# Kernel tuning notes

Measured on AMD Instinct MI355X. Metric: run time of the kernel, lower is better.

Reference implementation:

```python
import jax, jax.numpy as jnp
import numpy as np

B, N, D = 2, 2048, 512
H, VD = 8, 64  # v_dim = hid_dim / n_head


def setup_inputs() -> dict:
    key = jax.random.key(0)
    k1, k2, k3, k4 = jax.random.split(key, 4)
    inputs = jax.random.normal(k1, (B, N, D), dtype=jnp.float32)
    # lecun_normal: std = 1/sqrt(fan_in) with fan_in = D
    s = 1.0 / np.sqrt(D)
    q_w = jax.random.normal(k2, (H, D, VD), dtype=jnp.float32) * s
    k_w = jax.random.normal(k3, (H, D, VD), dtype=jnp.float32) * s
    v_w = jax.random.normal(k4, (H, D, VD), dtype=jnp.float32) * s
    return {"inputs": inputs, "q_w": q_w, "k_w": k_w, "v_w": v_w}


def reference(inputs, q_w, k_w, v_w):
    # QKV projections: [B,N,D] x [H,D,VD] -> [B,H,N,VD]
    q = jnp.einsum('bnj,hjk->bhnk', inputs, q_w)
    k = jnp.einsum('bnj,hjk->bhnk', inputs, k_w)
    v = jnp.einsum('bnj,hjk->bhnk', inputs, v_w)
    scale = 1.0 / jnp.sqrt(jnp.asarray(VD, dtype=q.dtype))
    scores = jnp.einsum('bhik,bhjk->bhij', q, k) * scale  # [B,H,N,N]
    att = jax.nn.softmax(scores, axis=-1)
    out = jnp.einsum('bhnj,bhjd->bhnd', att, v)  # [B,H,N,VD]
    out = jnp.transpose(out, (0, 2, 1, 3)).reshape(inputs.shape[0], -1, H * VD)  # [B,N,hid_dim]
    # keras GELU default is exact (non-approximate)
    return jax.nn.gelu(out, approximate=False)
```

## Files before the change

kernel.cpp:

```cpp
#include <hip/hip_runtime.h>
#include <hip/hip_bf16.h>
#include <math.h>

#define BB 2
#define NN 2048
#define DD 512
#define HH 8
#define VD 64

typedef _Float16 half8 __attribute__((ext_vector_type(8)));
typedef _Float16 half4 __attribute__((ext_vector_type(4)));
typedef __fp16 fp16x2 __attribute__((ext_vector_type(2)));
typedef float f32x4 __attribute__((ext_vector_type(4)));

#define GLDS16(gp, lp) __builtin_amdgcn_global_load_lds( \
    (const __attribute__((address_space(1))) void*)(gp), \
    (__attribute__((address_space(3))) void*)(lp), 16, 0, 0)

__device__ __forceinline__ float fexp2(float x) {
#if __has_builtin(__builtin_amdgcn_exp2f)
    return __builtin_amdgcn_exp2f(x);
#else
    return exp2f(x);
#endif
}

__device__ __forceinline__ void stage8(const _Float16* gsrc, size_t ldg, int r0,
                                       _Float16* lbase, int lane) {
    int r8 = lane >> 3;
    int ce = ((lane & 7) ^ r8) << 3;
    const _Float16* g = gsrc + (size_t)(r0 + r8) * ldg + ce;
    GLDS16(g, lbase);
}

__device__ __forceinline__ half8 frag_ld(const _Float16* tile, int row, int cb) {
    int off = row * 128 + (cb ^ ((row & 7) << 4));
    return *(const half8*)((const char*)tile + off);
}

__device__ __forceinline__ half8 frag_ldv(const _Float16* tile, int row, int cb) {
    int off = row * 256 + (cb ^ ((row & 15) << 4));
    return *(const half8*)((const char*)tile + off);
}

__device__ __forceinline__ float gelu_exact(float v) {
    return 0.5f * v * (1.f + erff(v * 0.70710678118654752f));
}

#define SM_BYTES 66560

__global__ __launch_bounds__(256) void k_prep(
    const float* __restrict__ x,
    const float* __restrict__ qw, const float* __restrict__ kw,
    const float* __restrict__ vw,
    _Float16* __restrict__ wt, _Float16* __restrict__ xh)
{
    __shared__ __align__(16) float ls[64][65];
    const int bid = blockIdx.x, t = threadIdx.x;
#pragma unroll
    for (int j = 0; j < 2; ++j) {
        size_t idx = (((size_t)bid * 2 + j) * 256 + t) * 8;
        float4 a = *(const float4*)(x + idx);
        float4 b = *(const float4*)(x + idx + 4);
        half8 hv;
        hv[0] = (_Float16)a.x; hv[1] = (_Float16)a.y;
        hv[2] = (_Float16)a.z; hv[3] = (_Float16)a.w;
        hv[4] = (_Float16)b.x; hv[5] = (_Float16)b.y;
        hv[6] = (_Float16)b.z; hv[7] = (_Float16)b.w;
        *(half8*)(xh + idx) = hv;
    }
    if (bid < 192) {
        const int kc = bid & 7, h = (bid >> 3) & 7, ty = bid >> 6;
        const float* src = (ty == 0) ? qw : (ty == 1) ? kw : vw;
#pragma unroll
        for (int j = 0; j < 4; ++j) {
            int idx = t + 256 * j;
            int k = idx >> 4, o4 = idx & 15;
            float4 v = *(const float4*)(src + ((size_t)(h * DD + kc * 64 + k) * VD + o4 * 4));
            ls[k][o4 * 4 + 0] = v.x; ls[k][o4 * 4 + 1] = v.y;
            ls[k][o4 * 4 + 2] = v.z; ls[k][o4 * 4 + 3] = v.w;
        }
        __syncthreads();
#pragma unroll
        for (int j = 0; j < 4; ++j) {
            int idx = t + 256 * j;
            int o = idx >> 4, k4 = idx & 15;
            half4 hv;
#pragma unroll
            for (int i = 0; i < 4; ++i) hv[i] = (_Float16)ls[k4 * 4 + i][o];
            *(half4*)(wt + ((size_t)(ty * HH + h) * VD + o) * DD + kc * 64 + k4 * 4) = hv;
        }
    }
}

__global__ __launch_bounds__(256) void k_proj(
    const _Float16* __restrict__ xh,
    const _Float16* __restrict__ wt,
    _Float16* __restrict__ qsp,
    _Float16* __restrict__ kbp,
    _Float16* __restrict__ vtp)
{
    __shared__ __align__(16) _Float16 xls[2][4096];
    __shared__ __align__(16) _Float16 wls[2][12288];
    const int bid = blockIdx.x, t = threadIdx.x;
    const int wave = t >> 6, lane = t & 63;
    const int lq = lane & 15, g = lane >> 4;
    const int h = bid & 7;
    const int m0 = (bid >> 3) * 64;
    const int rbase = 32 * (wave >> 1);
    const int cbase = 96 * (wave & 1);

    f32x4 acc[2][6];
#pragma unroll
    for (int a = 0; a < 2; ++a)
#pragma unroll
        for (int c = 0; c < 6; ++c) acc[a][c] = (f32x4){0.f, 0.f, 0.f, 0.f};

    auto stage = [&](int buf, int ks) {
#pragma unroll
        for (int j = 0; j < 2; ++j) {
            int i = wave * 2 + j;
            stage8(xh + (size_t)m0 * DD + ks * 64, DD, i * 8, &xls[buf][i * 512], lane);
        }
#pragma unroll
        for (int j = 0; j < 6; ++j) {
            int i = wave * 6 + j;
            int ty = i >> 3;
            int ol = (i & 7) * 8;
            stage8(wt + ((size_t)(ty * HH + h) * VD + ol) * DD + ks * 64, DD, 0,
                   &wls[buf][i * 512], lane);
        }
    };

    stage(0, 0);
    stage(1, 1);
    for (int ks = 0; ks < 8; ++ks) {
        const int buf = ks & 1;
        if (ks < 7) asm volatile("s_waitcnt vmcnt(8)" ::: "memory");
        else        asm volatile("s_waitcnt vmcnt(0)" ::: "memory");
        __builtin_amdgcn_s_barrier();
        half8 af[2][2];
        half8 bf[6][2];
#pragma unroll
        for (int amt = 0; amt < 2; ++amt) {
            af[amt][0] = frag_ld(xls[buf], rbase + amt * 16 + lq, 16 * g);
            af[amt][1] = frag_ld(xls[buf], rbase + amt * 16 + lq, 64 + 16 * g);
        }
#pragma unroll
        for (int ct = 0; ct < 6; ++ct) {
            int wr = cbase + ct * 16 + lq;
            bf[ct][0] = frag_ld(wls[buf], wr, 16 * g);
            bf[ct][1] = frag_ld(wls[buf], wr, 64 + 16 * g);
        }
        asm volatile("s_waitcnt lgkmcnt(0)" ::: "memory");
        __builtin_amdgcn_sched_barrier(0);
        __builtin_amdgcn_s_barrier();
        if (ks + 2 < 8) stage(buf, ks + 2);
        __builtin_amdgcn_s_setprio(1);
#pragma unroll
        for (int ct = 0; ct < 6; ++ct) {
#pragma unroll
            for (int amt = 0; amt < 2; ++amt) {
                acc[amt][ct] = __builtin_amdgcn_mfma_f32_16x16x32_f16(af[amt][0], bf[ct][0], acc[amt][ct], 0, 0, 0);
                acc[amt][ct] = __builtin_amdgcn_mfma_f32_16x16x32_f16(af[amt][1], bf[ct][1], acc[amt][ct], 0, 0, 0);
            }
        }
        __builtin_amdgcn_s_setprio(0);
    }

    const int b0 = m0 >> 11;
    const int nb0 = m0 & (NN - 1);
    const size_t bh = (size_t)(b0 * HH + h);
    _Float16* ldsA = &wls[0][0];
    _Float16* ldsV = &wls[0][0];
    const int rn = t >> 2;
    const int rc = t & 3;

    __syncthreads();
    if ((wave & 1) == 0) {
#pragma unroll
        for (int ct = 0; ct < 4; ++ct) {
            int o = ct * 16 + lq;
#pragma unroll
            for (int amt = 0; amt < 2; ++amt)
#pragma unroll
                for (int i = 0; i < 4; ++i) {
                    int n = rbase + amt * 16 + 4 * g + i;
                    ldsA[n * 72 + o] = (_Float16)(acc[amt][ct][i] * 0.18033688011112042f);
                }
        }
    }
    __syncthreads();
    {
        half8 v0 = *(const half8*)&ldsA[rn * 72 + rc * 16];
        half8 v1 = *(const half8*)&ldsA[rn * 72 + rc * 16 + 8];
        _Float16* qp = qsp + (bh * NN + nb0 + rn) * VD + rc * 16;
        *(half8*)qp = v0;
        *(half8*)(qp + 8) = v1;
    }

    __syncthreads();
    if ((wave & 1) == 0) {
#pragma unroll
        for (int ct = 4; ct < 6; ++ct) {
            int o = (ct - 4) * 16 + lq;
#pragma unroll
            for (int amt = 0; amt < 2; ++amt)
#pragma unroll
                for (int i = 0; i < 4; ++i) {
                    int n = rbase + amt * 16 + 4 * g + i;
                    ldsA[n * 72 + o] = (_Float16)acc[amt][ct][i];
                }
        }
    } else {
#pragma unroll
        for (int ct = 0; ct < 2; ++ct) {
            int o = 32 + ct * 16 + lq;
#pragma unroll
            for (int amt = 0; amt < 2; ++amt)
#pragma unroll
                for (int i = 0; i < 4; ++i) {
                    int n = rbase + amt * 16 + 4 * g + i;
                    ldsA[n * 72 + o] = (_Float16)acc[amt][ct][i];
                }
        }
    }
    __syncthreads();
    {
        half8 v0 = *(const half8*)&ldsA[rn * 72 + rc * 16];
        half8 v1 = *(const half8*)&ldsA[rn * 72 + rc * 16 + 8];
        _Float16* kp = kbp + (bh * NN + nb0 + rn) * VD + rc * 16;
        *(half8*)kp = v0;
        *(half8*)(kp + 8) = v1;
    }

    __syncthreads();
    if (wave & 1) {
#pragma unroll
        for (int ct = 2; ct < 6; ++ct) {
            int o = (ct - 2) * 16 + lq;
#pragma unroll
            for (int amt = 0; amt < 2; ++amt) {
                int n0 = rbase + amt * 16 + 4 * g;
                half4 hv;
#pragma unroll
                for (int i = 0; i < 4; ++i) hv[i] = (_Float16)acc[amt][ct][i];
                *(half4*)&ldsV[o * 88 + n0] = hv;
            }
        }
    }
    __syncthreads();
    {
#pragma unroll
        for (int blk = 0; blk < 2; ++blk) {
            half4 lo = *(const half4*)&ldsV[rn * 88 + 32 * blk + 4 * rc];
            half4 hi = *(const half4*)&ldsV[rn * 88 + 32 * blk + 16 + 4 * rc];
            half8 pk;
            pk[0] = lo[0]; pk[1] = lo[1]; pk[2] = lo[2]; pk[3] = lo[3];
            pk[4] = hi[0]; pk[5] = hi[1]; pk[6] = hi[2]; pk[7] = hi[3];
            *(half8*)(vtp + (bh * VD + rn) * NN + nb0 + 32 * blk + 8 * rc) = pk;
        }
    }
}

__global__ __launch_bounds__(256, 2) void k_attn(
    const _Float16* __restrict__ qs,
    const _Float16* __restrict__ kb,
    const _Float16* __restrict__ vt,
    float* __restrict__ out)
{
    constexpr int NITER = NN / 128;
    __shared__ __align__(16) char SM[SM_BYTES];
    const int bid = blockIdx.x, t = threadIdx.x;
    const int wave = t >> 6, lane = t & 63;
    const int lq = lane & 15, g = lane >> 4;
    const int xcd = bid & 7;
    const int bh = xcd * 2 + ((bid >> 3) & 1);
    const int qt = bid >> 4;
    const int qbase = qt * 64;

    half8 qf[4][2];
#pragma unroll
    for (int qg = 0; qg < 4; ++qg)
#pragma unroll
        for (int ds = 0; ds < 2; ++ds)
            qf[qg][ds] = *(const half8*)(qs + ((size_t)bh * NN + qbase + 16 * qg + lq) * VD + 32 * ds + 8 * g);

    const int r8 = lane >> 3;
    const _Float16* kS = kb + ((size_t)bh * NN + 32 * wave + r8) * VD + 8 * ((lane & 7) ^ r8);
    const _Float16* vS[4];
#pragma unroll
    for (int uu = 0; uu < 4; ++uu) {
        int vrow = 16 * wave + 4 * uu + g;
        vS[uu] = vt + ((size_t)bh * VD + vrow) * NN + 8 * (lq ^ (vrow & 15));
    }

    _Float16* kb0 = (_Float16*)(SM);
    _Float16* vb0 = (_Float16*)(SM + 16384);
    _Float16* kb1 = (_Float16*)(SM + 32768);
    _Float16* vb1 = (_Float16*)(SM + 49152);

    auto stage = [&](int b, int j) {
        _Float16* kd = (b ? kb1 : kb0) + 4 * wave * 512;
        const _Float16* kp = kS + (size_t)j * 128 * VD;
#pragma unroll
        for (int uu = 0; uu < 4; ++uu)
            GLDS16(kp + uu * 8 * VD, kd + uu * 512);
        _Float16* vd = (b ? vb1 : vb0) + 4 * wave * 512;
#pragma unroll
        for (int uu = 0; uu < 4; ++uu)
            GLDS16(vS[uu] + j * 128, vd + uu * 512);
    };

    f32x4 oacc[4][4];
    f32x4 oacc_l[4];
#pragma unroll
    for (int qg = 0; qg < 4; ++qg) {
#pragma unroll
        for (int dt = 0; dt < 4; ++dt) oacc[qg][dt] = (f32x4){0.f, 0.f, 0.f, 0.f};
        oacc_l[qg] = (f32x4){0.f, 0.f, 0.f, 0.f};
    }
    half8 vones;
#pragma unroll
    for (int i = 0; i < 8; ++i) vones[i] = (_Float16)1.0f;

    stage(0, 0);
    stage(1, 1);

    union PU { fp16x2 h2[4]; half8 h8; };

    for (int j = 0; j < NITER; ++j) {
        const int b = j & 1;
        if (j < NITER - 1) asm volatile("s_waitcnt vmcnt(8)" ::: "memory");
        else               asm volatile("s_waitcnt vmcnt(0)" ::: "memory");
        __builtin_amdgcn_s_barrier();
        const _Float16* kB = b ? kb1 : kb0;
        const _Float16* vB = b ? vb1 : vb0;
        half8 kf[2][2], vf[4];
#pragma unroll
        for (int mt = 0; mt < 2; ++mt)
#pragma unroll
            for (int ds = 0; ds < 2; ++ds)
                kf[mt][ds] = frag_ld(kB, 32 * wave + 16 * mt + lq, 64 * ds + 16 * g);
#pragma unroll
        for (int dt = 0; dt < 4; ++dt)
            vf[dt] = frag_ldv(vB, 16 * dt + lq, 64 * wave + 16 * g);
        asm volatile("s_waitcnt lgkmcnt(0)" ::: "memory");
        __builtin_amdgcn_sched_barrier(0);
        __builtin_amdgcn_s_barrier();
        if (j + 2 < NITER) stage(b, j + 2);
        f32x4 sc[2][2];
        __builtin_amdgcn_s_setprio(1);
#pragma unroll
        for (int mt = 0; mt < 2; ++mt) {
            sc[0][mt] = (f32x4){0.f, 0.f, 0.f, 0.f};
            sc[0][mt] = __builtin_amdgcn_mfma_f32_16x16x32_f16(kf[mt][0], qf[0][0], sc[0][mt], 0, 0, 0);
            sc[0][mt] = __builtin_amdgcn_mfma_f32_16x16x32_f16(kf[mt][1], qf[0][1], sc[0][mt], 0, 0, 0);
        }
#pragma unroll
        for (int qg = 0; qg < 4; ++qg) {
            const int cur = qg & 1;
            if (qg < 3) {
#pragma unroll
                for (int mt = 0; mt < 2; ++mt) {
                    sc[cur ^ 1][mt] = (f32x4){0.f, 0.f, 0.f, 0.f};
                    sc[cur ^ 1][mt] = __builtin_amdgcn_mfma_f32_16x16x32_f16(kf[mt][0], qf[qg + 1][0], sc[cur ^ 1][mt], 0, 0, 0);
                    sc[cur ^ 1][mt] = __builtin_amdgcn_mfma_f32_16x16x32_f16(kf[mt][1], qf[qg + 1][1], sc[cur ^ 1][mt], 0, 0, 0);
                }
            }
            PU pu;
            {
                float p00 = fexp2(sc[cur][0][0]);
                float p01 = fexp2(sc[cur][0][1]);
                float p02 = fexp2(sc[cur][0][2]);
                float p03 = fexp2(sc[cur][0][3]);
                float p10 = fexp2(sc[cur][1][0]);
                float p11 = fexp2(sc[cur][1][1]);
                float p12 = fexp2(sc[cur][1][2]);
                float p13 = fexp2(sc[cur][1][3]);
                pu.h2[0] = __builtin_amdgcn_cvt_pkrtz(p00, p01);
                pu.h2[1] = __builtin_amdgcn_cvt_pkrtz(p02, p03);
                pu.h2[2] = __builtin_amdgcn_cvt_pkrtz(p10, p11);
                pu.h2[3] = __builtin_amdgcn_cvt_pkrtz(p12, p13);
            }
#pragma unroll
            for (int dt = 0; dt < 4; ++dt)
                oacc[qg][dt] = __builtin_amdgcn_mfma_f32_16x16x32_f16(vf[dt], pu.h8, oacc[qg][dt], 0, 0, 0);
            oacc_l[qg] = __builtin_amdgcn_mfma_f32_16x16x32_f16(vones, pu.h8, oacc_l[qg], 0, 0, 0);
        }
        __builtin_amdgcn_s_setprio(0);
    }

    float* lsm  = (float*)(SM + 65536);
    float* sred = (float*)SM;
    __syncthreads();
    if (g == 0) {
#pragma unroll
        for (int qg = 0; qg < 4; ++qg) lsm[wave * 64 + 16 * qg + lq] = oacc_l[qg][0];
    }
#pragma unroll
    for (int qg = 0; qg < 4; ++qg)
#pragma unroll
        for (int dt = 0; dt < 4; ++dt)
            *(f32x4*)(sred + (size_t)wave * 4096 + (16 * qg + lq) * 64 + 16 * dt + 4 * g) = oacc[qg][dt];
    __syncthreads();
    const int b2 = bh >> 3, h = bh & 7;
    const int q = t >> 2, cg2 = t & 3;
    float lt = (lsm[q] + lsm[64 + q]) + (lsm[128 + q] + lsm[192 + q]);
    float inv = 1.f / lt;
    float* op = out + ((size_t)b2 * NN + qbase + q) * (HH * VD) + h * VD + 16 * cg2;
#pragma unroll
    for (int c2 = 0; c2 < 4; ++c2) {
        int off = q * 64 + 16 * cg2 + 4 * c2;
        f32x4 o = *(const f32x4*)(sred + off);
        o += *(const f32x4*)(sred + 4096 + off);
        o += *(const f32x4*)(sred + 8192 + off);
        o += *(const f32x4*)(sred + 12288 + off);
        float4 r;
        r.x = gelu_exact(o[0] * inv);
        r.y = gelu_exact(o[1] * inv);
        r.z = gelu_exact(o[2] * inv);
        r.w = gelu_exact(o[3] * inv);
        *(float4*)(op + 4 * c2) = r;
    }
}

extern "C" void kernel_launch(void* const* d_in, const int* in_sizes, int n_in,
                              void* d_out, int out_size, void* d_ws, size_t ws_size,
                              hipStream_t stream)
{
    const float* x  = (const float*)d_in[0];
    const float* qw = (const float*)d_in[1];
    const float* kw = (const float*)d_in[2];
    const float* vw = (const float*)d_in[3];
    float* out = (float*)d_out;

    _Float16* wt  = (_Float16*)d_ws;
    _Float16* xhp = wt  + 786432;
    _Float16* qsp = xhp + 2097152;
    _Float16* kbp = qsp + 2097152;
    _Float16* vtp = kbp + 2097152;

    hipLaunchKernelGGL(k_prep, dim3(512), dim3(256), 0, stream,
                       x, qw, kw, vw, wt, xhp);
    hipLaunchKernelGGL(k_proj, dim3(512), dim3(256), 0, stream,
                       xhp, wt, qsp, kbp, vtp);
    hipLaunchKernelGGL(k_attn, dim3(512), dim3(256), 0, stream,
                       qsp, kbp, vtp, out);
}
```

Measured before the change: 49.96 us.

## Load K/V fragments directly from global into registers, dropping LDS staging

The attention main loop stops staging K and V tiles through LDS with global_load_lds and barriers. Each wave now loads its own K and V MFMA fragments straight from global memory into two register sets that alternate, and the loop is fully unrolled. This is meant to remove LDS round trips and the two block barriers per iteration. In exchange it uses more registers, issues smaller strided global loads whose latency must be hidden by the register double buffer, and loses the swizzled bank-conflict-free layout.

New measurement: 59.82 us. 1.2x slower.

```diff
diff --git a/kernel.cpp b/kernel.cpp
--- a/kernel.cpp
+++ b/kernel.cpp
@@ -35,11 +35,6 @@
 
 __device__ __forceinline__ half8 frag_ld(const _Float16* tile, int row, int cb) {
     int off = row * 128 + (cb ^ ((row & 7) << 4));
-    return *(const half8*)((const char*)tile + off);
-}
-
-__device__ __forceinline__ half8 frag_ldv(const _Float16* tile, int row, int cb) {
-    int off = row * 256 + (cb ^ ((row & 15) << 4));
     return *(const half8*)((const char*)tile + off);
 }
 
@@ -286,31 +281,8 @@
         for (int ds = 0; ds < 2; ++ds)
             qf[qg][ds] = *(const half8*)(qs + ((size_t)bh * NN + qbase + 16 * qg + lq) * VD + 32 * ds + 8 * g);
 
-    const int r8 = lane >> 3;
-    const _Float16* kS = kb + ((size_t)bh * NN + 32 * wave + r8) * VD + 8 * ((lane & 7) ^ r8);
-    const _Float16* vS[4];
-#pragma unroll
-    for (int uu = 0; uu < 4; ++uu) {
-        int vrow = 16 * wave + 4 * uu + g;
-        vS[uu] = vt + ((size_t)bh * VD + vrow) * NN + 8 * (lq ^ (vrow & 15));
-    }
-
-    _Float16* kb0 = (_Float16*)(SM);
-    _Float16* vb0 = (_Float16*)(SM + 16384);
-    _Float16* kb1 = (_Float16*)(SM + 32768);
-    _Float16* vb1 = (_Float16*)(SM + 49152);
-
-    auto stage = [&](int b, int j) {
-        _Float16* kd = (b ? kb1 : kb0) + 4 * wave * 512;
-        const _Float16* kp = kS + (size_t)j * 128 * VD;
-#pragma unroll
-        for (int uu = 0; uu < 4; ++uu)
-            GLDS16(kp + uu * 8 * VD, kd + uu * 512);
-        _Float16* vd = (b ? vb1 : vb0) + 4 * wave * 512;
-#pragma unroll
-        for (int uu = 0; uu < 4; ++uu)
-            GLDS16(vS[uu] + j * 128, vd + uu * 512);
-    };
+    const _Float16* kP = kb + ((size_t)bh * NN + 32 * wave + lq) * VD + 8 * g;
+    const _Float16* vP = vt + ((size_t)bh * VD + lq) * NN + 32 * wave + 8 * g;
 
     f32x4 oacc[4][4];
     f32x4 oacc_l[4];
@@ -324,72 +296,70 @@
 #pragma unroll
     for (int i = 0; i < 8; ++i) vones[i] = (_Float16)1.0f;
 
-    stage(0, 0);
-    stage(1, 1);
-
     union PU { fp16x2 h2[4]; half8 h8; };
 
-    for (int j = 0; j < NITER; ++j) {
-        const int b = j & 1;
-        if (j < NITER - 1) asm volatile("s_waitcnt vmcnt(8)" ::: "memory");
-        else               asm volatile("s_waitcnt vmcnt(0)" ::: "memory");
-        __builtin_amdgcn_s_barrier();
-        const _Float16* kB = b ? kb1 : kb0;
-        const _Float16* vB = b ? vb1 : vb0;
-        half8 kf[2][2], vf[4];
-#pragma unroll
-        for (int mt = 0; mt < 2; ++mt)
-#pragma unroll
-            for (int ds = 0; ds < 2; ++ds)
-                kf[mt][ds] = frag_ld(kB, 32 * wave + 16 * mt + lq, 64 * ds + 16 * g);
-#pragma unroll
-        for (int dt = 0; dt < 4; ++dt)
-            vf[dt] = frag_ldv(vB, 16 * dt + lq, 64 * wave + 16 * g);
-        asm volatile("s_waitcnt lgkmcnt(0)" ::: "memory");
-        __builtin_amdgcn_sched_barrier(0);
-        __builtin_amdgcn_s_barrier();
-        if (j + 2 < NITER) stage(b, j + 2);
-        f32x4 sc[2][2];
-        __builtin_amdgcn_s_setprio(1);
-#pragma unroll
-        for (int mt = 0; mt < 2; ++mt) {
-            sc[0][mt] = (f32x4){0.f, 0.f, 0.f, 0.f};
-            sc[0][mt] = __builtin_amdgcn_mfma_f32_16x16x32_f16(kf[mt][0], qf[0][0], sc[0][mt], 0, 0, 0);
-            sc[0][mt] = __builtin_amdgcn_mfma_f32_16x16x32_f16(kf[mt][1], qf[0][1], sc[0][mt], 0, 0, 0);
-        }
-#pragma unroll
-        for (int qg = 0; qg < 4; ++qg) {
-            const int cur = qg & 1;
-            if (qg < 3) {
-#pragma unroll
-                for (int mt = 0; mt < 2; ++mt) {
-                    sc[cur ^ 1][mt] = (f32x4){0.f, 0.f, 0.f, 0.f};
-                    sc[cur ^ 1][mt] = __builtin_amdgcn_mfma_f32_16x16x32_f16(kf[mt][0], qf[qg + 1][0], sc[cur ^ 1][mt], 0, 0, 0);
-                    sc[cur ^ 1][mt] = __builtin_amdgcn_mfma_f32_16x16x32_f16(kf[mt][1], qf[qg + 1][1], sc[cur ^ 1][mt], 0, 0, 0);
-                }
-            }
-            PU pu;
-            {
-                float p00 = fexp2(sc[cur][0][0]);
-                float p01 = fexp2(sc[cur][0][1]);
-                float p02 = fexp2(sc[cur][0][2]);
-                float p03 = fexp2(sc[cur][0][3]);
-                float p10 = fexp2(sc[cur][1][0]);
-                float p11 = fexp2(sc[cur][1][1]);
-                float p12 = fexp2(sc[cur][1][2]);
-                float p13 = fexp2(sc[cur][1][3]);
-                pu.h2[0] = __builtin_amdgcn_cvt_pkrtz(p00, p01);
-                pu.h2[1] = __builtin_amdgcn_cvt_pkrtz(p02, p03);
-                pu.h2[2] = __builtin_amdgcn_cvt_pkrtz(p10, p11);
-                pu.h2[3] = __builtin_amdgcn_cvt_pkrtz(p12, p13);
-            }
-#pragma unroll
-            for (int dt = 0; dt < 4; ++dt)
-                oacc[qg][dt] = __builtin_amdgcn_mfma_f32_16x16x32_f16(vf[dt], pu.h8, oacc[qg][dt], 0, 0, 0);
-            oacc_l[qg] = __builtin_amdgcn_mfma_f32_16x16x32_f16(vones, pu.h8, oacc_l[qg], 0, 0, 0);
-        }
-        __builtin_amdgcn_s_setprio(0);
-    }
+#define LOADK(DST, J)                                                            \
+    _Pragma("unroll") for (int mt = 0; mt < 2; ++mt)                             \
+        _Pragma("unroll") for (int ds = 0; ds < 2; ++ds)                         \
+            DST[mt][ds] = *(const half8*)(kP + ((size_t)(J) * 128 + mt * 16) * VD + ds * 32);
+
+#define LOADV(DST, J)                                                            \
+    _Pragma("unroll") for (int dt = 0; dt < 4; ++dt)                             \
+        DST[dt] = *(const half8*)(vP + (size_t)dt * 16 * NN + (J) * 128);
+
+#define AT_COMP(KF, VF)                                                          \
+    {                                                                            \
+        f32x4 sc[2][2];                                                          \
+        __builtin_amdgcn_s_setprio(1);                                           \
+        _Pragma("unroll") for (int mt = 0; mt < 2; ++mt) {                       \
+            sc[0][mt] = (f32x4){0.f, 0.f, 0.f, 0.f};                             \
+            sc[0][mt] = __builtin_amdgcn_mfma_f32_16x16x32_f16(KF[mt][0], qf[0][0], sc[0][mt], 0, 0, 0); \
+            sc[0][mt] = __builtin_amdgcn_mfma_f32_16x16x32_f16(KF[mt][1], qf[0][1], sc[0][mt], 0, 0, 0); \
+        }                                                                        \
+        _Pragma("unroll") for (int qg = 0; qg < 4; ++qg) {                       \
+            const int cur = qg & 1;                                              \
+            if (qg < 3) {                                                        \
+                _Pragma("unroll") for (int mt = 0; mt < 2; ++mt) {               \
+                    sc[cur ^ 1][mt] = (f32x4){0.f, 0.f, 0.f, 0.f};               \
+                    sc[cur ^ 1][mt] = __builtin_amdgcn_mfma_f32_16x16x32_f16(KF[mt][0], qf[qg + 1][0], sc[cur ^ 1][mt], 0, 0, 0); \
+                    sc[cur ^ 1][mt] = __builtin_amdgcn_mfma_f32_16x16x32_f16(KF[mt][1], qf[qg + 1][1], sc[cur ^ 1][mt], 0, 0, 0); \
+                }                                                                \
+            }                                                                    \
+            PU pu;                                                               \
+            {                                                                    \
+                float p00 = fexp2(sc[cur][0][0]);                                \
+                float p01 = fexp2(sc[cur][0][1]);                                \
+                float p02 = fexp2(sc[cur][0][2]);                                \
+                float p03 = fexp2(sc[cur][0][3]);                                \
+                float p10 = fexp2(sc[cur][1][0]);                                \
+                float p11 = fexp2(sc[cur][1][1]);                                \
+                float p12 = fexp2(sc[cur][1][2]);                                \
+                float p13 = fexp2(sc[cur][1][3]);                                \
+                pu.h2[0] = __builtin_amdgcn_cvt_pkrtz(p00, p01);                 \
+                pu.h2[1] = __builtin_amdgcn_cvt_pkrtz(p02, p03);                 \
+                pu.h2[2] = __builtin_amdgcn_cvt_pkrtz(p10, p11);                 \
+                pu.h2[3] = __builtin_amdgcn_cvt_pkrtz(p12, p13);                 \
+            }                                                                    \
+            _Pragma("unroll") for (int dt = 0; dt < 4; ++dt)                     \
+                oacc[qg][dt] = __builtin_amdgcn_mfma_f32_16x16x32_f16(VF[dt], pu.h8, oacc[qg][dt], 0, 0, 0); \
+            oacc_l[qg] = __builtin_amdgcn_mfma_f32_16x16x32_f16(vones, pu.h8, oacc_l[qg], 0, 0, 0); \
+        }                                                                        \
+        __builtin_amdgcn_s_setprio(0);                                           \
+    }
+
+    half8 kfA[2][2], vfA[4], kfB[2][2], vfB[4];
+    LOADK(kfA, 0); LOADV(vfA, 0);
+    LOADK(kfB, 1); LOADV(vfB, 1);
+#pragma unroll
+    for (int j = 0; j < NITER; j += 2) {
+        AT_COMP(kfA, vfA);
+        if (j + 2 < NITER) { LOADK(kfA, j + 2); LOADV(vfA, j + 2); }
+        AT_COMP(kfB, vfB);
+        if (j + 3 < NITER) { LOADK(kfB, j + 3); LOADV(vfB, j + 3); }
+    }
+#undef AT_COMP
+#undef LOADV
+#undef LOADK
 
     float* lsm  = (float*)(SM + 65536);
     float* sred = (float*)SM;
```
